# Performance work log

Measured on AMD Instinct MI355X. Metric: run time of the kernel, lower is better.

Reference implementation:

```python
import jax, jax.numpy as jnp
import numpy as np

NEG_INF = -1e6  # d2l masked_softmax fill value


def setup_inputs() -> dict:
    key = jax.random.key(0)
    kq, kk, kv, kl = jax.random.split(key, 4)
    n, s, d = 32, 2048, 64
    queries = jax.random.normal(kq, (n, s, d), dtype=jnp.float32)
    keys = jax.random.normal(kk, (n, s, d), dtype=jnp.float32)
    values = jax.random.normal(kv, (n, s, d), dtype=jnp.float32)
    valid_lens = jax.random.randint(kl, (n,), 1, s + 1, dtype=jnp.int32)
    return {"queries": queries, "keys": keys, "values": values, "valid_lens": valid_lens}


def reference(queries, keys, values, valid_lens):
    d = queries.shape[-1]
    # scores: [n, q, k]
    scores = jnp.einsum("nqd,nkd->nqk", queries, keys) / jnp.sqrt(jnp.float32(d))
    kv_len = scores.shape[-1]
    # masked_softmax: positions >= valid_len get NEG_INF before softmax
    mask = jnp.arange(kv_len, dtype=jnp.int32)[None, None, :] < valid_lens[:, None, None]
    scores = jnp.where(mask, scores, NEG_INF)
    attn = jax.nn.softmax(scores, axis=-1)
    # dropout rate 0.0 (inference) -> identity
    return jnp.einsum("nqk,nkd->nqd", attn, values)
```

## Files before the change

### kernel.cpp

```cpp
#include <hip/hip_runtime.h>
#include <hip/hip_bf16.h>


typedef short bf16x8 __attribute__((ext_vector_type(8)));
typedef float f32x4  __attribute__((ext_vector_type(4)));
typedef unsigned int u32;
typedef u32 u32x2 __attribute__((ext_vector_type(2)));
typedef u32 u32x4 __attribute__((ext_vector_type(4)));

#define SEQ 2048
#define DH 64
#define BK 64
#define LDSP 72
#define SCLQ 0.18033688011112042f

static __device__ __forceinline__ short f2bf(float f) {
    unsigned u = __float_as_uint(f);
    return (short)((u + 0x7FFFu + ((u >> 16) & 1u)) >> 16);
}
static __device__ __forceinline__ u32 pk2bf(float lo, float hi) {
    __hip_bfloat162 h = __float22bfloat162_rn(float2{lo, hi});
    return *(u32*)&h;
}

__global__ __launch_bounds__(256, 4)
void prepass(const float* __restrict__ K, const float* __restrict__ V,
             short* __restrict__ Kbf, short* __restrict__ Vt)
{
    __shared__ short T[DH][LDSP];

    const int tid  = threadIdx.x;
    const int wave = tid >> 6;
    const int lane = tid & 63;
    const int b  = blockIdx.x & 31;
    const int kt = blockIdx.x >> 5;
    const int k0 = kt * BK;
    const size_t bo = (size_t)b * SEQ * DH;

    const float* Ks = K + bo + (size_t)k0 * DH;
    u32* Kd = (u32*)(Kbf + bo + (size_t)k0 * DH);
    #pragma unroll
    for (int h = 0; h < 2; ++h) {
        const int c2 = tid + h * 256;
        f32x4 a = *(const f32x4*)(Ks + c2 * 8);
        f32x4 c = *(const f32x4*)(Ks + c2 * 8 + 4);
        u32x4 o;
        o[0] = pk2bf(a[0], a[1]); o[1] = pk2bf(a[2], a[3]);
        o[2] = pk2bf(c[0], c[1]); o[3] = pk2bf(c[2], c[3]);
        *(u32x4*)(Kd + c2 * 4) = o;
    }

    #pragma unroll
    for (int h = 0; h < 2; ++h) {
        const int d0 = wave * 8 + h * 32;
        const float* src = V + bo + (size_t)(k0 + lane) * DH + d0;
        f32x4 va = *(const f32x4*)(src);
        f32x4 vb = *(const f32x4*)(src + 4);
        #pragma unroll
        for (int j = 0; j < 4; ++j) {
            T[d0 + j][lane]     = f2bf(va[j]);
            T[d0 + 4 + j][lane] = f2bf(vb[j]);
        }
    }
    __syncthreads();

    short* Vd = Vt + (size_t)b * DH * SEQ;
    #pragma unroll
    for (int h = 0; h < 2; ++h) {
        const int c2 = tid + h * 256;
        const int d  = c2 >> 3;
        const int kc = (c2 & 7) * 8;
        *(bf16x8*)(Vd + (size_t)d * SEQ + k0 + kc) = *(const bf16x8*)(&T[d][kc]);
    }
}

template <bool PRE>
__global__ __launch_bounds__(256, 4)
void attn_fwd(const float* __restrict__ Q,
              const float* __restrict__ Kf, const float* __restrict__ Vf,
              const short* __restrict__ Kbf, const short* __restrict__ Vtg,
              const int* __restrict__ VL, float* __restrict__ O)
{
    __shared__ short Klds[BK][LDSP];
    __shared__ short Vt[DH][LDSP];
    __shared__ short Pw[4][16][LDSP];
    __shared__ int   Rsort[32];

    const int tid  = threadIdx.x;
    const int wave = tid >> 6;
    const int lane = tid & 63;
    const int g    = lane >> 4;
    const int l15  = lane & 15;

    if (tid < 32) {
        const int nv = (VL[tid] + BK - 1) >> 6;
        int rank = 0;
        for (int jj = 0; jj < 32; ++jj) {
            const int nj = (VL[jj] + BK - 1) >> 6;
            rank += (nj > nv) || (nj == nv && jj < tid);
        }
        Rsort[rank] = tid;
    }
    __syncthreads();

    const int jb = blockIdx.x & 255;
    const int sl = blockIdx.x >> 8;
    const int c8 = jb >> 5;
    const int qt = jb & 31;
    const int rk = (sl == 0) ? c8 : (sl == 1) ? (15 - c8)
                 : (sl == 2) ? (16 + c8) : (31 - c8);
    const int b  = Rsort[rk];

    const int vl  = VL[b];
    const int nkt = (vl + BK - 1) >> 6;

    const size_t bo = (size_t)b * SEQ * DH;
    const short* Kb = Kbf + bo;
    const short* Vb = Vtg + (size_t)b * DH * SEQ;
    const float* Kbf32 = Kf + bo;
    const float* Vbf32 = Vf + bo;

    const int qrow = qt * 64 + wave * 16 + l15;
    bf16x8 aq0, aq1;
    {
        const float* qp = Q + bo + (size_t)qrow * DH + g * 8;
        f32x4 q0 = *(const f32x4*)(qp);
        f32x4 q1 = *(const f32x4*)(qp + 4);
        f32x4 q2 = *(const f32x4*)(qp + 32);
        f32x4 q3 = *(const f32x4*)(qp + 36);
        #pragma unroll
        for (int j = 0; j < 4; ++j) {
            aq0[j]     = f2bf(q0[j] * SCLQ);
            aq0[j + 4] = f2bf(q1[j] * SCLQ);
            aq1[j]     = f2bf(q2[j] * SCLQ);
            aq1[j + 4] = f2bf(q3[j] * SCLQ);
        }
    }

    bf16x8 ones;
    #pragma unroll
    for (int j = 0; j < 8; ++j) ones[j] = (short)0x3F80;

    f32x4 oacc[4];
    #pragma unroll
    for (int i = 0; i < 4; ++i) oacc[i] = f32x4{0.f, 0.f, 0.f, 0.f};
    f32x4 lacc = f32x4{0.f, 0.f, 0.f, 0.f};

    bf16x8 kpre[2], vpre[2];
    f32x4 kpre32[4], vpre32[4];
    if (PRE) {
        #pragma unroll
        for (int h = 0; h < 2; ++h) {
            const int c2 = tid + h * 256;
            kpre[h] = *(const bf16x8*)(Kb + c2 * 8);
            vpre[h] = *(const bf16x8*)(Vb + (size_t)(c2 >> 3) * SEQ + ((c2 & 7) * 8));
        }
    } else {
        #pragma unroll
        for (int h = 0; h < 4; ++h) {
            const int cc = tid + h * 256;
            kpre32[h] = *(const f32x4*)(Kbf32 + (size_t)(cc >> 4) * DH + (cc & 15) * 4);
        }
        #pragma unroll
        for (int h = 0; h < 2; ++h) {
            const float* src = Vbf32 + (size_t)lane * DH + wave * 8 + h * 32;
            vpre32[2 * h]     = *(const f32x4*)(src);
            vpre32[2 * h + 1] = *(const f32x4*)(src + 4);
        }
    }

    for (int kt = 0; kt < nkt; ++kt) {
        const int k0 = kt * BK;

        if (PRE) {
            #pragma unroll
            for (int h = 0; h < 2; ++h) {
                const int c2 = tid + h * 256;
                *(bf16x8*)(&Klds[c2 >> 3][(c2 & 7) * 8]) = kpre[h];
                *(bf16x8*)(&Vt[c2 >> 3][(c2 & 7) * 8])   = vpre[h];
            }
        } else {
            #pragma unroll
            for (int h = 0; h < 4; ++h) {
                const int cc = tid + h * 256;
                u32x2 o;
                o[0] = pk2bf(kpre32[h][0], kpre32[h][1]);
                o[1] = pk2bf(kpre32[h][2], kpre32[h][3]);
                *(u32x2*)(&Klds[cc >> 4][(cc & 15) * 4]) = o;
            }
            #pragma unroll
            for (int h = 0; h < 2; ++h) {
                const int d0 = wave * 8 + h * 32;
                #pragma unroll
                for (int j = 0; j < 4; ++j) {
                    Vt[d0 + j][lane]     = f2bf(vpre32[2 * h][j]);
                    Vt[d0 + 4 + j][lane] = f2bf(vpre32[2 * h + 1][j]);
                }
            }
        }
        __syncthreads();

        if (kt + 1 < nkt) {
            const int kn = k0 + BK;
            if (PRE) {
                #pragma unroll
                for (int h = 0; h < 2; ++h) {
                    const int c2 = tid + h * 256;
                    kpre[h] = *(const bf16x8*)(Kb + (size_t)kn * DH + c2 * 8);
                    vpre[h] = *(const bf16x8*)(Vb + (size_t)(c2 >> 3) * SEQ + kn + ((c2 & 7) * 8));
                }
            } else {
                #pragma unroll
                for (int h = 0; h < 4; ++h) {
                    const int cc = tid + h * 256;
                    kpre32[h] = *(const f32x4*)(Kbf32 + (size_t)(kn + (cc >> 4)) * DH + (cc & 15) * 4);
                }
                #pragma unroll
                for (int h = 0; h < 2; ++h) {
                    const float* src = Vbf32 + (size_t)(kn + lane) * DH + wave * 8 + h * 32;
                    vpre32[2 * h]     = *(const f32x4*)(src);
                    vpre32[2 * h + 1] = *(const f32x4*)(src + 4);
                }
            }
        }

        f32x4 s[4];
        #pragma unroll
        for (int nb = 0; nb < 4; ++nb) {
            bf16x8 ak0 = *(const bf16x8*)(&Klds[nb * 16 + l15][g * 8]);
            bf16x8 ak1 = *(const bf16x8*)(&Klds[nb * 16 + l15][32 + g * 8]);
            f32x4 acc = f32x4{0.f, 0.f, 0.f, 0.f};
            acc = __builtin_amdgcn_mfma_f32_16x16x32_bf16(ak0, aq0, acc, 0, 0, 0);
            acc = __builtin_amdgcn_mfma_f32_16x16x32_bf16(ak1, aq1, acc, 0, 0, 0);
            s[nb] = acc;
        }

        if (k0 + BK <= vl) {
            #pragma unroll
            for (int nb = 0; nb < 4; ++nb)
                #pragma unroll
                for (int r = 0; r < 4; ++r)
                    s[nb][r] = __builtin_amdgcn_exp2f(s[nb][r]);
        } else {
            #pragma unroll
            for (int nb = 0; nb < 4; ++nb)
                #pragma unroll
                for (int r = 0; r < 4; ++r) {
                    const bool ok = (k0 + nb * 16 + g * 4 + r) < vl;
                    s[nb][r] = ok ? __builtin_amdgcn_exp2f(s[nb][r]) : 0.f;
                }
        }

        #pragma unroll
        for (int nb = 0; nb < 4; ++nb) {
            u32x2 pkv;
            pkv[0] = pk2bf(s[nb][0], s[nb][1]);
            pkv[1] = pk2bf(s[nb][2], s[nb][3]);
            *(u32x2*)(&Pw[wave][l15][nb * 16 + g * 4]) = pkv;
        }
        asm volatile("" ::: "memory");

        #pragma unroll
        for (int cc = 0; cc < 2; ++cc) {
            bf16x8 ap = *(const bf16x8*)(&Pw[wave][l15][cc * 32 + g * 8]);
            lacc = __builtin_amdgcn_mfma_f32_16x16x32_bf16(ap, ones, lacc, 0, 0, 0);
            #pragma unroll
            for (int db = 0; db < 4; ++db) {
                bf16x8 bv = *(const bf16x8*)(&Vt[db * 16 + l15][cc * 32 + g * 8]);
                oacc[db] = __builtin_amdgcn_mfma_f32_16x16x32_bf16(ap, bv, oacc[db], 0, 0, 0);
            }
        }
        __syncthreads();
    }

    #pragma unroll
    for (int r = 0; r < 4; ++r) {
        const float inv = 1.0f / lacc[r];
        const int row = qt * 64 + wave * 16 + g * 4 + r;
        #pragma unroll
        for (int db = 0; db < 4; ++db)
            O[bo + (size_t)row * DH + db * 16 + l15] = oacc[db][r] * inv;
    }
}

extern "C" void kernel_launch(void* const* d_in, const int* in_sizes, int n_in,
                              void* d_out, int out_size, void* d_ws, size_t ws_size,
                              hipStream_t stream) {
    const float* Q  = (const float*)d_in[0];
    const float* K  = (const float*)d_in[1];
    const float* V  = (const float*)d_in[2];
    const int*   VL = (const int*)d_in[3];
    float* O = (float*)d_out;

    const size_t nel = (size_t)32 * SEQ * DH;
    const size_t need = 2 * nel * sizeof(short);
    if (ws_size >= need) {
        short* Kbf = (short*)d_ws;
        short* Vt  = Kbf + nel;
        prepass<<<dim3(1024), dim3(256), 0, stream>>>(K, V, Kbf, Vt);
        attn_fwd<true><<<dim3(1024), dim3(256), 0, stream>>>(Q, K, V, Kbf, Vt, VL, O);
    } else {
        attn_fwd<false><<<dim3(1024), dim3(256), 0, stream>>>(Q, K, V, nullptr, nullptr, VL, O);
    }
}
```

Before: 127.7 us.

## Load K/V MFMA fragments directly from global bf16 buffers, dropping LDS staging

Result: slower. 220.0 us (+72.2%).

```diff
diff --git a/kernel.cpp b/kernel.cpp
--- a/kernel.cpp
+++ b/kernel.cpp
@@ -74,15 +74,11 @@
     }
 }
 
-template <bool PRE>
 __global__ __launch_bounds__(256, 4)
 void attn_fwd(const float* __restrict__ Q,
-              const float* __restrict__ Kf, const float* __restrict__ Vf,
               const short* __restrict__ Kbf, const short* __restrict__ Vtg,
               const int* __restrict__ VL, float* __restrict__ O)
 {
-    __shared__ short Klds[BK][LDSP];
-    __shared__ short Vt[DH][LDSP];
     __shared__ short Pw[4][16][LDSP];
     __shared__ int   Rsort[32];
 
@@ -117,8 +113,6 @@
     const size_t bo = (size_t)b * SEQ * DH;
     const short* Kb = Kbf + bo;
     const short* Vb = Vtg + (size_t)b * DH * SEQ;
-    const float* Kbf32 = Kf + bo;
-    const float* Vbf32 = Vf + bo;
 
     const int qrow = qt * 64 + wave * 16 + l15;
     bf16x8 aq0, aq1;
@@ -146,83 +140,144 @@
     for (int i = 0; i < 4; ++i) oacc[i] = f32x4{0.f, 0.f, 0.f, 0.f};
     f32x4 lacc = f32x4{0.f, 0.f, 0.f, 0.f};
 
-    bf16x8 kpre[2], vpre[2];
-    f32x4 kpre32[4], vpre32[4];
-    if (PRE) {
-        #pragma unroll
-        for (int h = 0; h < 2; ++h) {
-            const int c2 = tid + h * 256;
-            kpre[h] = *(const bf16x8*)(Kb + c2 * 8);
-            vpre[h] = *(const bf16x8*)(Vb + (size_t)(c2 >> 3) * SEQ + ((c2 & 7) * 8));
-        }
-    } else {
+    const short* KbL = Kb + (size_t)l15 * DH + g * 8;
+    const short* VbL = Vb + (size_t)l15 * SEQ + g * 8;
+
+    for (int kt = 0; kt < nkt; ++kt) {
+        const int k0 = kt * BK;
+
+        bf16x8 kf[8];
+        #pragma unroll
+        for (int nb = 0; nb < 4; ++nb) {
+            const short* kp = KbL + (size_t)(k0 + nb * 16) * DH;
+            kf[nb * 2 + 0] = *(const bf16x8*)(kp);
+            kf[nb * 2 + 1] = *(const bf16x8*)(kp + 32);
+        }
+        bf16x8 vf[8];
+        #pragma unroll
+        for (int db = 0; db < 4; ++db) {
+            const short* vp = VbL + (size_t)(db * 16) * SEQ + k0;
+            vf[db * 2 + 0] = *(const bf16x8*)(vp);
+            vf[db * 2 + 1] = *(const bf16x8*)(vp + 32);
+        }
+
+        f32x4 s[4];
+        #pragma unroll
+        for (int nb = 0; nb < 4; ++nb) {
+            f32x4 acc = f32x4{0.f, 0.f, 0.f, 0.f};
+            acc = __builtin_amdgcn_mfma_f32_16x16x32_bf16(kf[nb * 2 + 0], aq0, acc, 0, 0, 0);
+            acc = __builtin_amdgcn_mfma_f32_16x16x32_bf16(kf[nb * 2 + 1], aq1, acc, 0, 0, 0);
+            s[nb] = acc;
+        }
+
+        if (k0 + BK <= vl) {
+            #pragma unroll
+            for (int nb = 0; nb < 4; ++nb)
+                #pragma unroll
+                for (int r = 0; r < 4; ++r)
+                    s[nb][r] = __builtin_amdgcn_exp2f(s[nb][r]);
+        } else {
+            #pragma unroll
+            for (int nb = 0; nb < 4; ++nb)
+                #pragma unroll
+                for (int r = 0; r < 4; ++r) {
+                    const bool ok = (k0 + nb * 16 + g * 4 + r) < vl;
+                    s[nb][r] = ok ? __builtin_amdgcn_exp2f(s[nb][r]) : 0.f;
+                }
+        }
+
+        #pragma unroll
+        for (int nb = 0; nb < 4; ++nb) {
+            u32x2 pkv;
+            pkv[0] = pk2bf(s[nb][0], s[nb][1]);
+            pkv[1] = pk2bf(s[nb][2], s[nb][3]);
+            *(u32x2*)(&Pw[wave][l15][nb * 16 + g * 4]) = pkv;
+        }
+        asm volatile("" ::: "memory");
+
+        #pragma unroll
+        for (int cc = 0; cc < 2; ++cc) {
+            bf16x8 ap = *(const bf16x8*)(&Pw[wave][l15][cc * 32 + g * 8]);
+            lacc = __builtin_amdgcn_mfma_f32_16x16x32_bf16(ap, ones, lacc, 0, 0, 0);
+            #pragma unroll
+            for (int db = 0; db < 4; ++db)
+                oacc[db] = __builtin_amdgcn_mfma_f32_16x16x32_bf16(ap, vf[db * 2 + cc], oacc[db], 0, 0, 0);
+        }
+    }
+
+    #pragma unroll
+    for (int r = 0; r < 4; ++r) {
+        const float inv = 1.0f / lacc[r];
+        const int row = qt * 64 + wave * 16 + g * 4 + r;
+        #pragma unroll
+        for (int db = 0; db < 4; ++db)
+            O[bo + (size_t)row * DH + db * 16 + l15] = oacc[db][r] * inv;
+    }
+}
+
+__global__ __launch_bounds__(256, 4)
+void attn_fwd_fb(const float* __restrict__ Q, const float* __restrict__ Kf,
+                 const float* __restrict__ Vf, const int* __restrict__ VL,
+                 float* __restrict__ O)
+{
+    __shared__ short Klds[BK][LDSP];
+    __shared__ short Vt[DH][LDSP];
+    __shared__ short Pw[4][16][LDSP];
+
+    const int tid  = threadIdx.x;
+    const int wave = tid >> 6;
+    const int lane = tid & 63;
+    const int g    = lane >> 4;
+    const int l15  = lane & 15;
+    const int b  = blockIdx.x & 31;
+    const int qt = blockIdx.x >> 5;
+    const int vl  = VL[b];
+    const int nkt = (vl + BK - 1) >> 6;
+    const size_t bo = (size_t)b * SEQ * DH;
+
+    const int qrow = qt * 64 + wave * 16 + l15;
+    bf16x8 aq0, aq1;
+    {
+        const float* qp = Q + bo + (size_t)qrow * DH + g * 8;
+        f32x4 q0 = *(const f32x4*)(qp);
+        f32x4 q1 = *(const f32x4*)(qp + 4);
+        f32x4 q2 = *(const f32x4*)(qp + 32);
+        f32x4 q3 = *(const f32x4*)(qp + 36);
+        #pragma unroll
+        for (int j = 0; j < 4; ++j) {
+            aq0[j] = f2bf(q0[j] * SCLQ); aq0[j + 4] = f2bf(q1[j] * SCLQ);
+            aq1[j] = f2bf(q2[j] * SCLQ); aq1[j + 4] = f2bf(q3[j] * SCLQ);
+        }
+    }
+    bf16x8 ones;
+    #pragma unroll
+    for (int j = 0; j < 8; ++j) ones[j] = (short)0x3F80;
+    f32x4 oacc[4];
+    #pragma unroll
+    for (int i = 0; i < 4; ++i) oacc[i] = f32x4{0.f, 0.f, 0.f, 0.f};
+    f32x4 lacc = f32x4{0.f, 0.f, 0.f, 0.f};
+
+    for (int kt = 0; kt < nkt; ++kt) {
+        const int k0 = kt * BK;
         #pragma unroll
         for (int h = 0; h < 4; ++h) {
             const int cc = tid + h * 256;
-            kpre32[h] = *(const f32x4*)(Kbf32 + (size_t)(cc >> 4) * DH + (cc & 15) * 4);
+            f32x4 v = *(const f32x4*)(Kf + bo + (size_t)(k0 + (cc >> 4)) * DH + (cc & 15) * 4);
+            u32x2 o; o[0] = pk2bf(v[0], v[1]); o[1] = pk2bf(v[2], v[3]);
+            *(u32x2*)(&Klds[cc >> 4][(cc & 15) * 4]) = o;
         }
         #pragma unroll
         for (int h = 0; h < 2; ++h) {
-            const float* src = Vbf32 + (size_t)lane * DH + wave * 8 + h * 32;
-            vpre32[2 * h]     = *(const f32x4*)(src);
-            vpre32[2 * h + 1] = *(const f32x4*)(src + 4);
-        }
-    }
-
-    for (int kt = 0; kt < nkt; ++kt) {
-        const int k0 = kt * BK;
-
-        if (PRE) {
-            #pragma unroll
-            for (int h = 0; h < 2; ++h) {
-                const int c2 = tid + h * 256;
-                *(bf16x8*)(&Klds[c2 >> 3][(c2 & 7) * 8]) = kpre[h];
-                *(bf16x8*)(&Vt[c2 >> 3][(c2 & 7) * 8])   = vpre[h];
+            const int d0 = wave * 8 + h * 32;
+            const float* src = Vf + bo + (size_t)(k0 + lane) * DH + d0;
+            f32x4 va = *(const f32x4*)(src);
+            f32x4 vb = *(const f32x4*)(src + 4);
+            #pragma unroll
+            for (int j = 0; j < 4; ++j) {
+                Vt[d0 + j][lane] = f2bf(va[j]); Vt[d0 + 4 + j][lane] = f2bf(vb[j]);
             }
-        } else {
-            #pragma unroll
-            for (int h = 0; h < 4; ++h) {
-                const int cc = tid + h * 256;
-                u32x2 o;
-                o[0] = pk2bf(kpre32[h][0], kpre32[h][1]);
-                o[1] = pk2bf(kpre32[h][2], kpre32[h][3]);
-                *(u32x2*)(&Klds[cc >> 4][(cc & 15) * 4]) = o;
-            }
-            #pragma unroll
-            for (int h = 0; h < 2; ++h) {
-                const int d0 = wave * 8 + h * 32;
-                #pragma unroll
-                for (int j = 0; j < 4; ++j) {
-                    Vt[d0 + j][lane]     = f2bf(vpre32[2 * h][j]);
-                    Vt[d0 + 4 + j][lane] = f2bf(vpre32[2 * h + 1][j]);
-                }
-            }
         }
         __syncthreads();
-
-        if (kt + 1 < nkt) {
-            const int kn = k0 + BK;
-            if (PRE) {
-                #pragma unroll
-                for (int h = 0; h < 2; ++h) {
-                    const int c2 = tid + h * 256;
-                    kpre[h] = *(const bf16x8*)(Kb + (size_t)kn * DH + c2 * 8);
-                    vpre[h] = *(const bf16x8*)(Vb + (size_t)(c2 >> 3) * SEQ + kn + ((c2 & 7) * 8));
-                }
-            } else {
-                #pragma unroll
-                for (int h = 0; h < 4; ++h) {
-                    const int cc = tid + h * 256;
-                    kpre32[h] = *(const f32x4*)(Kbf32 + (size_t)(kn + (cc >> 4)) * DH + (cc & 15) * 4);
-                }
-                #pragma unroll
-                for (int h = 0; h < 2; ++h) {
-                    const float* src = Vbf32 + (size_t)(kn + lane) * DH + wave * 8 + h * 32;
-                    vpre32[2 * h]     = *(const f32x4*)(src);
-                    vpre32[2 * h + 1] = *(const f32x4*)(src + 4);
-                }
-            }
-        }
 
         f32x4 s[4];
         #pragma unroll
@@ -234,23 +289,13 @@
             acc = __builtin_amdgcn_mfma_f32_16x16x32_bf16(ak1, aq1, acc, 0, 0, 0);
             s[nb] = acc;
         }
-
-        if (k0 + BK <= vl) {
-            #pragma unroll
-            for (int nb = 0; nb < 4; ++nb)
-                #pragma unroll
-                for (int r = 0; r < 4; ++r)
-                    s[nb][r] = __builtin_amdgcn_exp2f(s[nb][r]);
-        } else {
-            #pragma unroll
-            for (int nb = 0; nb < 4; ++nb)
-                #pragma unroll
-                for (int r = 0; r < 4; ++r) {
-                    const bool ok = (k0 + nb * 16 + g * 4 + r) < vl;
-                    s[nb][r] = ok ? __builtin_amdgcn_exp2f(s[nb][r]) : 0.f;
-                }
-        }
-
+        #pragma unroll
+        for (int nb = 0; nb < 4; ++nb)
+            #pragma unroll
+            for (int r = 0; r < 4; ++r) {
+                const bool ok = (k0 + nb * 16 + g * 4 + r) < vl;
+                s[nb][r] = ok ? __builtin_amdgcn_exp2f(s[nb][r]) : 0.f;
+            }
         #pragma unroll
         for (int nb = 0; nb < 4; ++nb) {
             u32x2 pkv;
@@ -259,7 +304,6 @@
             *(u32x2*)(&Pw[wave][l15][nb * 16 + g * 4]) = pkv;
         }
         asm volatile("" ::: "memory");
-
         #pragma unroll
         for (int cc = 0; cc < 2; ++cc) {
             bf16x8 ap = *(const bf16x8*)(&Pw[wave][l15][cc * 32 + g * 8]);
@@ -272,7 +316,6 @@
         }
         __syncthreads();
     }
-
     #pragma unroll
     for (int r = 0; r < 4; ++r) {
         const float inv = 1.0f / lacc[r];
@@ -298,8 +341,8 @@
         short* Kbf = (short*)d_ws;
         short* Vt  = Kbf + nel;
         prepass<<<dim3(1024), dim3(256), 0, stream>>>(K, V, Kbf, Vt);
-        attn_fwd<true><<<dim3(1024), dim3(256), 0, stream>>>(Q, K, V, Kbf, Vt, VL, O);
+        attn_fwd<<<dim3(1024), dim3(256), 0, stream>>>(Q, Kbf, Vt, VL, O);
     } else {
-        attn_fwd<false><<<dim3(1024), dim3(256), 0, stream>>>(Q, K, V, nullptr, nullptr, VL, O);
-    }
-}
+        attn_fwd_fb<<<dim3(1024), dim3(256), 0, stream>>>(Q, K, V, VL, O);
+    }
+}
```
